# Kernel optimization log

Hardware: AMD Instinct MI355X
Metric: run time of the kernel (lower is better)

## Reference

```python
import jax, jax.numpy as jnp
import numpy as np

BINS = 64
VMIN, VMAX = 0.0, 1.0


def _calc_histogram(x):
    # x: [B, C, H, W] float
    B, C, H, W = x.shape
    x_norm = jnp.clip((x - VMIN) / (VMAX - VMIN), 0.0, 1.0)
    flat = x_norm.reshape(B * C, H * W)
    # torch.histc semantics over [0,1]: bin i = [i/BINS, (i+1)/BINS), last bin closed.
    idx = jnp.clip((flat * BINS).astype(jnp.int32), 0, BINS - 1)  # [B*C, HW]
    row_offset = (jnp.arange(B * C, dtype=jnp.int32) * BINS)[:, None]
    flat_idx = (idx + row_offset).reshape(-1)
    counts = jax.ops.segment_sum(
        jnp.ones(flat_idx.shape, dtype=x.dtype), flat_idx,
        num_segments=B * C * BINS,
    ).reshape(B * C, BINS)
    counts = counts / jnp.clip(counts.sum(axis=1, keepdims=True), 1e-8, None)
    return counts.reshape(B, C, BINS)


def reference(fake_images, real_images):
    hist_fake = _calc_histogram(fake_images)
    hist_real = _calc_histogram(real_images)
    # loss_type == 'l1'
    return jnp.abs(hist_fake - hist_real).mean()


def setup_inputs() -> dict:
    key = jax.random.key(0)
    k1, k2 = jax.random.split(key)
    shape = (32, 3, 512, 512)
    fake_images = jax.random.uniform(k1, shape, dtype=jnp.float32)
    real_images = jax.random.uniform(k2, shape, dtype=jnp.float32)
    return {"fake_images": fake_images, "real_images": real_images}
```

## Files before the change

### kernel.cpp

```cpp
#include <hip/hip_runtime.h>
#include <hip/hip_bf16.h>


#define HW        262144
#define ROWS      96
#define NBINS     64
#define BPR       8
#define CHUNK     (HW / BPR)
#define THREADS   256
#define F4_ITERS  (CHUNK / 4 / THREADS)
#define NBLOCKS   (2 * ROWS * BPR)
#define NREG      64
#define PITCH     65
#define PRIV_W    (NREG * PITCH)

__global__ __launch_bounds__(THREADS)
void hist_kernel(const float* __restrict__ fake,
                 const float* __restrict__ real,
                 unsigned int* __restrict__ partial) {
    __shared__ unsigned int priv[PRIV_W];
    __shared__ unsigned int comb[4][NBINS];

    const int tid  = threadIdx.x;
    const int lane = tid & 63;
    const int wv   = tid >> 6;

    for (int k = tid; k < PRIV_W; k += THREADS) priv[k] = 0u;
    __syncthreads();

    const int b     = blockIdx.x;
    const int chunk = b & (BPR - 1);
    const int rowg  = b >> 3;
    const float* src = (rowg < ROWS) ? fake : real;
    const int row    = (rowg < ROWS) ? rowg : (rowg - ROWS);

    const float4* __restrict__ p =
        (const float4*)(src + (size_t)row * HW + (size_t)chunk * CHUNK);

    unsigned int* __restrict__ reg = &priv[(tid >> 2) * PITCH];

#pragma unroll 4
    for (int i = 0; i < F4_ITERS; ++i) {
        float4 v = p[i * THREADS + tid];
        int b0 = min((int)(v.x * 64.0f), 63);
        int b1 = min((int)(v.y * 64.0f), 63);
        int b2 = min((int)(v.z * 64.0f), 63);
        int b3 = min((int)(v.w * 64.0f), 63);
        atomicAdd(&reg[b0], 1u);
        atomicAdd(&reg[b1], 1u);
        atomicAdd(&reg[b2], 1u);
        atomicAdd(&reg[b3], 1u);
    }
    __syncthreads();

    unsigned cnt = 0;
#pragma unroll
    for (int r = 0; r < 16; ++r)
        cnt += priv[(wv * 16 + r) * PITCH + lane];
    comb[wv][lane] = cnt;
    __syncthreads();

    if (tid < NBINS) {
        unsigned s = comb[0][tid] + comb[1][tid] + comb[2][tid] + comb[3][tid];
        partial[(size_t)b * NBINS + tid] = s;
    }
}

__global__ __launch_bounds__(1024)
void loss_kernel(const unsigned int* __restrict__ partial,
                 float* __restrict__ out) {
    const int tid = threadIdx.x;
    int acc = 0;
#pragma unroll
    for (int q = 0; q < 6; ++q) {
        const int pIdx = q * 1024 + tid;
        const int r  = pIdx >> 6;
        const int bb = pIdx & 63;
        unsigned cf = 0, cr = 0;
#pragma unroll
        for (int c = 0; c < BPR; ++c) {
            cf += partial[((r * BPR + c) * NBINS) + bb];
            cr += partial[(((ROWS + r) * BPR + c) * NBINS) + bb];
        }
        int d = (int)cf - (int)cr;
        acc += (d < 0) ? -d : d;
    }
#pragma unroll
    for (int off = 32; off > 0; off >>= 1)
        acc += __shfl_down(acc, off, 64);
    __shared__ int wsum[16];
    if ((tid & 63) == 0) wsum[tid >> 6] = acc;
    __syncthreads();
    if (tid == 0) {
        long long total = 0;
#pragma unroll
        for (int k = 0; k < 16; ++k) total += wsum[k];
        out[0] = (float)((double)total / (262144.0 * 6144.0));
    }
}

extern "C" void kernel_launch(void* const* d_in, const int* in_sizes, int n_in,
                              void* d_out, int out_size, void* d_ws, size_t ws_size,
                              hipStream_t stream) {
    const float* fake = (const float*)d_in[0];
    const float* real = (const float*)d_in[1];
    unsigned int* partial = (unsigned int*)d_ws;
    float* out = (float*)d_out;

    hist_kernel<<<NBLOCKS, THREADS, 0, stream>>>(fake, real, partial);
    loss_kernel<<<1, 1024, 0, stream>>>(partial, out);
}
```

Measured before the change: 219.9 us.

## Replace LDS atomic histogram with bit-sliced register counters and ballot reduction

Per-thread bin counts are now kept in eight 64-bit bit-planes in registers, one bit per bin per plane. Each float4 is folded in with a carry-save adder chain instead of four shared-memory atomics. At the end, a ballot and popcount per bin and per plane rebuild each wave's counts, which are then combined with a single LDS atomic per lane. This removes the LDS atomic traffic and bank contention in the hot loop. In exchange it adds about forty 64-bit logic ops per float4, and it relies on per-thread counts per bin staying below 256.

```diff
diff --git a/kernel.cpp b/kernel.cpp
--- a/kernel.cpp
+++ b/kernel.cpp
@@ -1,5 +1,4 @@
 #include <hip/hip_runtime.h>
-#include <hip/hip_bf16.h>
 
 
 #define HW        262144
@@ -10,22 +9,19 @@
 #define THREADS   256
 #define F4_ITERS  (CHUNK / 4 / THREADS)
 #define NBLOCKS   (2 * ROWS * BPR)
-#define NREG      64
-#define PITCH     65
-#define PRIV_W    (NREG * PITCH)
+
+typedef unsigned long long u64;
 
 __global__ __launch_bounds__(THREADS)
 void hist_kernel(const float* __restrict__ fake,
                  const float* __restrict__ real,
                  unsigned int* __restrict__ partial) {
-    __shared__ unsigned int priv[PRIV_W];
-    __shared__ unsigned int comb[4][NBINS];
+    __shared__ unsigned int bhist[NBINS];
 
     const int tid  = threadIdx.x;
     const int lane = tid & 63;
-    const int wv   = tid >> 6;
 
-    for (int k = tid; k < PRIV_W; k += THREADS) priv[k] = 0u;
+    if (tid < NBINS) bhist[tid] = 0u;
     __syncthreads();
 
     const int b     = blockIdx.x;
@@ -37,7 +33,7 @@
     const float4* __restrict__ p =
         (const float4*)(src + (size_t)row * HW + (size_t)chunk * CHUNK);
 
-    unsigned int* __restrict__ reg = &priv[(tid >> 2) * PITCH];
+    u64 p0 = 0, p1 = 0, p2 = 0, p3 = 0, p4 = 0, p5 = 0, p6 = 0, p7 = 0;
 
 #pragma unroll 4
     for (int i = 0; i < F4_ITERS; ++i) {
@@ -46,24 +42,53 @@
         int b1 = min((int)(v.y * 64.0f), 63);
         int b2 = min((int)(v.z * 64.0f), 63);
         int b3 = min((int)(v.w * 64.0f), 63);
-        atomicAdd(&reg[b0], 1u);
-        atomicAdd(&reg[b1], 1u);
-        atomicAdd(&reg[b2], 1u);
-        atomicAdd(&reg[b3], 1u);
+        u64 m0 = 1ull << b0, m1 = 1ull << b1;
+        u64 m2 = 1ull << b2, m3 = 1ull << b3;
+
+        u64 s1 = m0 ^ m1, c1 = m0 & m1;
+        u64 s2 = m2 ^ m3, c2 = m2 & m3;
+        u64 S  = s1 ^ s2, C  = s1 & s2;
+
+        u64 g0 = p0 & S;  p0 ^= S;
+
+        u64 u  = c1 ^ c2, vv = c1 & c2;
+        u64 s3 = u ^ C,   w  = u & C;
+        u64 t3 = vv | w;
+
+        u64 t  = s3 ^ g0;
+        u64 g1 = (p1 & t) | (s3 & g0);
+        p1 ^= t;
+
+        u64 t2 = t3 ^ g1;
+        u64 g2 = (p2 & t2) | (t3 & g1);
+        p2 ^= t2;
+
+        u64 g3 = p3 & g2; p3 ^= g2;
+        u64 g4 = p4 & g3; p4 ^= g3;
+        u64 g5 = p5 & g4; p5 ^= g4;
+        u64 g6 = p6 & g5; p6 ^= g5;
+        p7 ^= g6;
     }
+
+    unsigned mycnt = 0;
+#pragma unroll
+    for (int bb = 0; bb < NBINS; ++bb) {
+        unsigned ws =
+              (unsigned)__popcll(__ballot((unsigned)((p0 >> bb) & 1ull)))
+            + ((unsigned)__popcll(__ballot((unsigned)((p1 >> bb) & 1ull))) << 1)
+            + ((unsigned)__popcll(__ballot((unsigned)((p2 >> bb) & 1ull))) << 2)
+            + ((unsigned)__popcll(__ballot((unsigned)((p3 >> bb) & 1ull))) << 3)
+            + ((unsigned)__popcll(__ballot((unsigned)((p4 >> bb) & 1ull))) << 4)
+            + ((unsigned)__popcll(__ballot((unsigned)((p5 >> bb) & 1ull))) << 5)
+            + ((unsigned)__popcll(__ballot((unsigned)((p6 >> bb) & 1ull))) << 6)
+            + ((unsigned)__popcll(__ballot((unsigned)((p7 >> bb) & 1ull))) << 7);
+        if (lane == bb) mycnt = ws;
+    }
+    atomicAdd(&bhist[lane], mycnt);
     __syncthreads();
 
-    unsigned cnt = 0;
-#pragma unroll
-    for (int r = 0; r < 16; ++r)
-        cnt += priv[(wv * 16 + r) * PITCH + lane];
-    comb[wv][lane] = cnt;
-    __syncthreads();
-
-    if (tid < NBINS) {
-        unsigned s = comb[0][tid] + comb[1][tid] + comb[2][tid] + comb[3][tid];
-        partial[(size_t)b * NBINS + tid] = s;
-    }
+    if (tid < NBINS)
+        partial[(size_t)b * NBINS + tid] = bhist[tid];
 }
 
 __global__ __launch_bounds__(1024)
```

Measured after the change: 228.5 us. 3.9% more time.
